# Performance work log

Hardware: AMD Instinct MI355X
Metric: run time of the kernel (lower is better)

The kernel has to match this reference:

```python
import jax, jax.numpy as jnp
import numpy as np

TOP_K = 2
SCALING = 16.0 / 8.0  # alpha / rank


def setup_inputs() -> dict:
    key = jax.random.key(0)
    ks = jax.random.split(key, 9)
    B, V, D, P = 32, 21, 512, 64
    IN, OUT, E, R, H = D * P, 96, 8, 8, 256
    return {
        "x": jax.random.normal(ks[0], (B, V, D, P), jnp.float32),
        "W_base": jax.random.normal(ks[1], (OUT, IN), jnp.float32) * (IN ** -0.5),
        "b_base": jax.random.normal(ks[2], (OUT,), jnp.float32) * 0.01,
        "W1": jax.random.normal(ks[3], (H, D), jnp.float32) * (D ** -0.5),
        "b1": jax.random.normal(ks[4], (H,), jnp.float32) * 0.01,
        "W2": jax.random.normal(ks[5], (E, H), jnp.float32) * (H ** -0.5),
        "b2": jax.random.normal(ks[6], (E,), jnp.float32) * 0.01,
        "lora_A": jax.random.normal(ks[7], (E, R, IN), jnp.float32) * (IN ** -0.5),
        "lora_B": jax.random.normal(ks[8], (E, OUT, R), jnp.float32) * (R ** -0.5),
    }


def reference(x, W_base, b_base, W1, b1, W2, b2, lora_A, lora_B):
    B, V, D, P = x.shape
    E = lora_A.shape[0]
    # FlattenHead: flatten last two dims, then linear (dropout is identity in eval)
    flat = x.reshape(B, V, D * P)                      # [B, V, IN]
    base_out = flat @ W_base.T + b_base                # [B, V, OUT]
    # Router: pool over n_vars then patch dim -> [B, D]
    pooled = x.mean(axis=1).mean(axis=-1)
    h = jax.nn.relu(pooled @ W1.T + b1)
    logits = h @ W2.T + b2                             # [B, E]
    probs = jax.nn.softmax(logits, axis=-1)
    topw, topi = jax.lax.top_k(probs, TOP_K)           # [B, K]
    topw = topw / jnp.clip(topw.sum(-1, keepdims=True), 1e-6)
    # All LoRA experts (matches original dense compute), then weighted combine
    temp = jnp.einsum("bvi,eri->ebvr", flat, lora_A)   # [E, B, V, R]
    delta = jnp.einsum("ebvr,eor->ebvo", temp, lora_B) * SCALING  # [E, B, V, OUT]
    # Scatter top-k weights into dense [B, E] then combine (top-k sparse combine)
    w_full = jnp.zeros((B, E), x.dtype).at[jnp.arange(B)[:, None], topi].add(topw)
    moe_delta = jnp.einsum("be,ebvo->bvo", w_full, delta)
    return base_out + moe_delta, probs
```

## Files before the change

kernel.cpp:

```cpp
#include <hip/hip_runtime.h>

#define B_DIM 32
#define V_DIM 21
#define D_DIM 512
#define P_DIM 64
#define M_TOTAL 672
#define K_TOTAL 32768
#define OUT_DIM 96
#define E_DIM 8
#define R_DIM 8
#define H_DIM 256
#define N_TOTAL 160
#define SCALING 2.0f
#define POOL_SCALE (1.0f / (V_DIM * (float)P_DIM))

#define BM 64
#define BK 64
#define KSPLIT 64
#define K_PER_SPLIT (K_TOTAL / KSPLIT)
#define CHUNKS (K_PER_SPLIT / BK)
#define LDS_K (BK + 8)
#define SMN (M_TOTAL * N_TOTAL)
#define RC_ROWS 2

typedef __attribute__((ext_vector_type(4))) float floatx4;
typedef __attribute__((ext_vector_type(8))) short short8;
typedef __attribute__((ext_vector_type(4))) short shortx4;

__device__ __forceinline__ unsigned short f2bf(float f) {
  union { float f; unsigned int u; } v; v.f = f;
  unsigned int u = v.u + (0x7FFFu + ((v.u >> 16) & 1u));
  return (unsigned short)(u >> 16);
}

__global__ __launch_bounds__(256)
void convW_kernel(const float* __restrict__ W_base, const float* __restrict__ lora_A,
                  short* __restrict__ Wb, float* __restrict__ pooled) {
  int gid = blockIdx.x * 256 + threadIdx.x;
  if (blockIdx.x < 64) pooled[gid] = 0.0f;
  size_t base = (size_t)gid * 8;
  int row = (int)(base >> 15);
  int k = (int)(base & 32767);
  const float* src = (row < OUT_DIM) ? (W_base + ((size_t)row << 15) + k)
                                     : (lora_A + ((size_t)(row - OUT_DIM) << 15) + k);
  floatx4 v0 = ((const floatx4*)src)[0];
  floatx4 v1 = ((const floatx4*)src)[1];
  short8 sv;
  sv[0] = (short)f2bf(v0[0]); sv[1] = (short)f2bf(v0[1]);
  sv[2] = (short)f2bf(v0[2]); sv[3] = (short)f2bf(v0[3]);
  sv[4] = (short)f2bf(v1[0]); sv[5] = (short)f2bf(v1[1]);
  sv[6] = (short)f2bf(v1[2]); sv[7] = (short)f2bf(v1[3]);
  *(short8*)(Wb + base) = sv;
}

__global__ __launch_bounds__(256, 4)
void gemm_kernel(const float* __restrict__ x, const short* __restrict__ Wb,
                 float* __restrict__ P, float* __restrict__ pooled) {
  __shared__ short ldsA[BM * LDS_K];
  __shared__ short ldsB[N_TOTAL * LDS_K];
  __shared__ float lds_pool[5 * 8];
  const int tid = threadIdx.x;
  const int m0 = blockIdx.x * BM;
  const int ky = blockIdx.y;
  const int kbase = ky * K_PER_SPLIT;
  const int lane = tid & 63;
  const int wave = tid >> 6;
  const int quad = lane >> 4;
  const int l16 = lane & 15;
  const int b_first = m0 / V_DIM;
  const int d_first = kbase >> 6;

  if (tid < 40) lds_pool[tid] = 0.0f;

  floatx4 acc[10];
  #pragma unroll
  for (int nt = 0; nt < 10; ++nt) acc[nt] = (floatx4)(0.0f);

  floatx4 pa[4];
  short8 pb[5];

#define ISSUE(c)                                                                \
  {                                                                             \
    const int kc = kbase + (c) * BK;                                            \
    _Pragma("unroll")                                                           \
    for (int it = 0; it < 4; ++it) {                                            \
      int idx = it * 256 + tid;                                                 \
      int arow = idx >> 4;                                                      \
      int u = idx & 15;                                                         \
      int m = m0 + arow;                                                        \
      pa[it] = (m < M_TOTAL)                                                    \
          ? *(const floatx4*)(x + (size_t)m * K_TOTAL + kc + u * 4)             \
          : (floatx4)(0.0f);                                                    \
    }                                                                           \
    _Pragma("unroll")                                                           \
    for (int it = 0; it < 5; ++it) {                                            \
      int idx = it * 256 + tid;                                                 \
      int brow = idx >> 3;                                                      \
      int g = idx & 7;                                                          \
      pb[it] = *(const short8*)(Wb + (size_t)brow * K_TOTAL + kc + g * 8);      \
    }                                                                           \
  }

#define CONVERT_WRITE(c)                                                        \
  {                                                                             \
    _Pragma("unroll")                                                           \
    for (int it = 0; it < 4; ++it) {                                            \
      int idx = it * 256 + tid;                                                 \
      int arow = idx >> 4;                                                      \
      int u = idx & 15;                                                         \
      int m = m0 + arow;                                                        \
      floatx4 v = pa[it];                                                       \
         \
      float s = (v[0] + v[1]) + (v[2] + v[3]);                                  \
      s += __shfl_down(s, 8, 16);                                               \
      s += __shfl_down(s, 4, 16);                                               \
      s += __shfl_down(s, 2, 16);                                               \
      s += __shfl_down(s, 1, 16);                                               \
      if ((tid & 15) == 0 && m < M_TOTAL) {                                     \
        int b_local = (m / V_DIM) - b_first;                                    \
        atomicAdd(&lds_pool[b_local * 8 + (c)], s);                             \
      }                                                                         \
      shortx4 sv;                                                               \
      sv[0] = (short)f2bf(v[0]); sv[1] = (short)f2bf(v[1]);                     \
      sv[2] = (short)f2bf(v[2]); sv[3] = (short)f2bf(v[3]);                     \
      *(shortx4*)&ldsA[arow * LDS_K + u * 4] = sv;                              \
    }                                                                           \
    _Pragma("unroll")                                                           \
    for (int it = 0; it < 5; ++it) {                                            \
      int idx = it * 256 + tid;                                                 \
      int brow = idx >> 3;                                                      \
      int g = idx & 7;                                                          \
      *(short8*)&ldsB[brow * LDS_K + g * 8] = pb[it];                           \
    }                                                                           \
  }

  ISSUE(0);
  __syncthreads();
  CONVERT_WRITE(0);

  for (int c = 0; c < CHUNKS; ++c) {
    __syncthreads();
    if (c + 1 < CHUNKS) ISSUE(c + 1);
    #pragma unroll
    for (int ks = 0; ks < 2; ++ks) {
      const int ko = ks * 32 + quad * 8;
      short8 a = *(const short8*)&ldsA[(wave * 16 + l16) * LDS_K + ko];
      #pragma unroll
      for (int nt = 0; nt < 10; ++nt) {
        short8 b = *(const short8*)&ldsB[(nt * 16 + l16) * LDS_K + ko];
        acc[nt] = __builtin_amdgcn_mfma_f32_16x16x32_bf16(a, b, acc[nt], 0, 0, 0);
      }
    }
    __syncthreads();
    if (c + 1 < CHUNKS) CONVERT_WRITE(c + 1);
  }

  {
    const int mrow = m0 + wave * 16 + quad * 4;
    float* Pp = P + (size_t)ky * SMN + (size_t)mrow * N_TOTAL + l16;
    #pragma unroll
    for (int r = 0; r < 4; ++r)
      if (mrow + r < M_TOTAL)
        #pragma unroll
        for (int nt = 0; nt < 10; ++nt)
          Pp[(size_t)r * N_TOTAL + nt * 16] = acc[nt][r];
  }

  if (tid < 40) {
    int b = b_first + (tid >> 3);
    int d = d_first + (tid & 7);
    if (b < B_DIM)
      atomicAdd(&pooled[b * D_DIM + d], lds_pool[tid] * POOL_SCALE);
  }
}

__global__ __launch_bounds__(256)
void router_kernel(const float* __restrict__ pooled, const float* __restrict__ W1,
                   const float* __restrict__ b1, const float* __restrict__ W2,
                   const float* __restrict__ b2, float* __restrict__ wfull,
                   float* __restrict__ probs_out) {
  __shared__ float sp[D_DIM];
  __shared__ float sh[H_DIM];
  __shared__ float slog[E_DIM];
  const int b = blockIdx.x;
  const int t = threadIdx.x;
  sp[t] = pooled[b * D_DIM + t];
  sp[t + 256] = pooled[b * D_DIM + t + 256];
  __syncthreads();
  float acc = b1[t];
  const float* w1r = W1 + (size_t)t * D_DIM;
  for (int d = 0; d < D_DIM; ++d) acc += sp[d] * w1r[d];
  sh[t] = fmaxf(acc, 0.0f);
  __syncthreads();
  if (t < E_DIM) {
    float a = b2[t];
    const float* w2r = W2 + t * H_DIM;
    for (int j = 0; j < H_DIM; ++j) a += sh[j] * w2r[j];
    slog[t] = a;
  }
  __syncthreads();
  if (t == 0) {
    float p[E_DIM];
    float mx = slog[0];
    for (int e = 1; e < E_DIM; ++e) mx = fmaxf(mx, slog[e]);
    float se = 0.0f;
    for (int e = 0; e < E_DIM; ++e) { p[e] = __expf(slog[e] - mx); se += p[e]; }
    float inv = 1.0f / se;
    for (int e = 0; e < E_DIM; ++e) { p[e] *= inv; probs_out[b * E_DIM + e] = p[e]; }
    int i0 = 0;
    for (int e = 1; e < E_DIM; ++e) if (p[e] > p[i0]) i0 = e;
    int i1 = (i0 == 0) ? 1 : 0;
    for (int e = 0; e < E_DIM; ++e) if (e != i0 && p[e] > p[i1]) i1 = e;
    float s2 = p[i0] + p[i1];
    float invs = 1.0f / fmaxf(s2, 1e-6f);
    for (int e = 0; e < E_DIM; ++e) {
      float w = 0.0f;
      if (e == i0) w += p[i0] * invs;
      if (e == i1) w += p[i1] * invs;
      wfull[b * E_DIM + e] = w;
    }
  }
}

__global__ __launch_bounds__(256)
void reduce_combine_kernel(const float* __restrict__ P, const float* __restrict__ b_base,
                           const float* __restrict__ lora_B, const float* __restrict__ wfull,
                           float* __restrict__ out) {
  __shared__ float sS[RC_ROWS * N_TOTAL];
  const int t = threadIdx.x;
  const size_t base = (size_t)blockIdx.x * (RC_ROWS * N_TOTAL);
  for (int s = t; s < RC_ROWS * N_TOTAL; s += 256) {
    const float* Pp = P + base + s;
    float a = 0.0f;
    #pragma unroll 8
    for (int k = 0; k < KSPLIT; ++k) a += Pp[(size_t)k * SMN];
    sS[s] = a;
  }
  __syncthreads();
  if (t < RC_ROWS * OUT_DIM) {
    int mr = t / OUT_DIM;
    int o = t - mr * OUT_DIM;
    int mm = blockIdx.x * RC_ROWS + mr;
    int b = mm / V_DIM;
    const float* srow = sS + mr * N_TOTAL;
    float res = srow[o] + b_base[o];
    float moe = 0.0f;
    #pragma unroll
    for (int e = 0; e < E_DIM; ++e) {
      float we = wfull[b * E_DIM + e];
      if (we != 0.0f) {
        const float* lb = lora_B + ((size_t)e * OUT_DIM + o) * R_DIM;
        float dd = 0.0f;
        #pragma unroll
        for (int r = 0; r < R_DIM; ++r) dd += srow[OUT_DIM + e * R_DIM + r] * lb[r];
        moe += we * dd;
      }
    }
    out[(size_t)mm * OUT_DIM + o] = res + SCALING * moe;
  }
}

extern "C" void kernel_launch(void* const* d_in, const int* in_sizes, int n_in,
                              void* d_out, int out_size, void* d_ws, size_t ws_size,
                              hipStream_t stream) {
  const float* x      = (const float*)d_in[0];
  const float* W_base = (const float*)d_in[1];
  const float* b_base = (const float*)d_in[2];
  const float* W1     = (const float*)d_in[3];
  const float* b1     = (const float*)d_in[4];
  const float* W2     = (const float*)d_in[5];
  const float* b2     = (const float*)d_in[6];
  const float* lora_A = (const float*)d_in[7];
  const float* lora_B = (const float*)d_in[8];
  float* out = (float*)d_out;

  float* ws     = (float*)d_ws;
  float* pooled = ws;
  float* wfull  = ws + 16384;
  short* Wb     = (short*)(wfull + 256);
  float* P      = (float*)(Wb + (size_t)N_TOTAL * K_TOTAL);

  convW_kernel<<<(N_TOTAL * K_TOTAL / 8 + 255) / 256, 256, 0, stream>>>(
      W_base, lora_A, Wb, pooled);
  gemm_kernel<<<dim3(11, KSPLIT), 256, 0, stream>>>(x, Wb, P, pooled);
  router_kernel<<<B_DIM, 256, 0, stream>>>(pooled, W1, b1, W2, b2, wfull,
                                           out + (size_t)M_TOTAL * OUT_DIM);
  reduce_combine_kernel<<<M_TOTAL / RC_ROWS, 256, 0, stream>>>(
      P, b_base, lora_B, wfull, out);
}
```

Before: 205.5 us.

## Pre-convert x to bf16 in a separate pass and move pooling out of GEMM

Adds a combined conversion kernel that turns x into a bf16 workspace copy and computes the router's pooled means with atomics, alongside the existing weight conversion. The GEMM then loads bf16 x directly, with no in-loop conversion or pooling reduction, and the router now runs before the GEMM. This makes the GEMM main loop simpler and halves its A-operand load bytes. In exchange it adds an extra write and re-read of a bf16 copy of x, plus a memset.

```diff
diff --git a/kernel.cpp b/kernel.cpp
--- a/kernel.cpp
+++ b/kernel.cpp
@@ -23,9 +23,11 @@
 #define SMN (M_TOTAL * N_TOTAL)
 #define RC_ROWS 2
 
+#define XCONV_BLOCKS 10752
+#define WCONV_BLOCKS 2560
+
 typedef __attribute__((ext_vector_type(4))) float floatx4;
 typedef __attribute__((ext_vector_type(8))) short short8;
-typedef __attribute__((ext_vector_type(4))) short shortx4;
 
 __device__ __forceinline__ unsigned short f2bf(float f) {
   union { float f; unsigned int u; } v; v.f = f;
@@ -34,31 +36,55 @@
 }
 
 __global__ __launch_bounds__(256)
-void convW_kernel(const float* __restrict__ W_base, const float* __restrict__ lora_A,
-                  short* __restrict__ Wb, float* __restrict__ pooled) {
-  int gid = blockIdx.x * 256 + threadIdx.x;
-  if (blockIdx.x < 64) pooled[gid] = 0.0f;
-  size_t base = (size_t)gid * 8;
-  int row = (int)(base >> 15);
-  int k = (int)(base & 32767);
-  const float* src = (row < OUT_DIM) ? (W_base + ((size_t)row << 15) + k)
-                                     : (lora_A + ((size_t)(row - OUT_DIM) << 15) + k);
-  floatx4 v0 = ((const floatx4*)src)[0];
-  floatx4 v1 = ((const floatx4*)src)[1];
-  short8 sv;
-  sv[0] = (short)f2bf(v0[0]); sv[1] = (short)f2bf(v0[1]);
-  sv[2] = (short)f2bf(v0[2]); sv[3] = (short)f2bf(v0[3]);
-  sv[4] = (short)f2bf(v1[0]); sv[5] = (short)f2bf(v1[1]);
-  sv[6] = (short)f2bf(v1[2]); sv[7] = (short)f2bf(v1[3]);
-  *(short8*)(Wb + base) = sv;
+void conv_kernel(const float* __restrict__ x, const float* __restrict__ W_base,
+                 const float* __restrict__ lora_A, short* __restrict__ xb,
+                 short* __restrict__ Wb, float* __restrict__ pooled) {
+  const int tid = threadIdx.x;
+  if (blockIdx.x < XCONV_BLOCKS) {
+    size_t gid = (size_t)blockIdx.x * 256 + tid;
+    const int m = (int)(gid >> 12);
+    const int grp = (int)(gid & 4095);
+    const float* src = x + ((size_t)m << 15) + grp * 8;
+    floatx4 v0 = ((const floatx4*)src)[0];
+    floatx4 v1 = ((const floatx4*)src)[1];
+    short8 sv;
+    sv[0] = (short)f2bf(v0[0]); sv[1] = (short)f2bf(v0[1]);
+    sv[2] = (short)f2bf(v0[2]); sv[3] = (short)f2bf(v0[3]);
+    sv[4] = (short)f2bf(v1[0]); sv[5] = (short)f2bf(v1[1]);
+    sv[6] = (short)f2bf(v1[2]); sv[7] = (short)f2bf(v1[3]);
+    *(short8*)(xb + gid * 8) = sv;
+    float s = ((v0[0] + v0[1]) + (v0[2] + v0[3])) +
+              ((v1[0] + v1[1]) + (v1[2] + v1[3]));
+    s += __shfl_down(s, 4, 8);
+    s += __shfl_down(s, 2, 8);
+    s += __shfl_down(s, 1, 8);
+    if ((tid & 7) == 0) {
+      int b = m / V_DIM;
+      int d = grp >> 3;
+      atomicAdd(&pooled[b * D_DIM + d], s * POOL_SCALE);
+    }
+  } else {
+    size_t base = ((size_t)(blockIdx.x - XCONV_BLOCKS) * 256 + tid) * 8;
+    int row = (int)(base >> 15);
+    int k = (int)(base & 32767);
+    const float* src = (row < OUT_DIM) ? (W_base + ((size_t)row << 15) + k)
+                                       : (lora_A + ((size_t)(row - OUT_DIM) << 15) + k);
+    floatx4 v0 = ((const floatx4*)src)[0];
+    floatx4 v1 = ((const floatx4*)src)[1];
+    short8 sv;
+    sv[0] = (short)f2bf(v0[0]); sv[1] = (short)f2bf(v0[1]);
+    sv[2] = (short)f2bf(v0[2]); sv[3] = (short)f2bf(v0[3]);
+    sv[4] = (short)f2bf(v1[0]); sv[5] = (short)f2bf(v1[1]);
+    sv[6] = (short)f2bf(v1[2]); sv[7] = (short)f2bf(v1[3]);
+    *(short8*)(Wb + base) = sv;
+  }
 }
 
 __global__ __launch_bounds__(256, 4)
-void gemm_kernel(const float* __restrict__ x, const short* __restrict__ Wb,
-                 float* __restrict__ P, float* __restrict__ pooled) {
+void gemm_kernel(const short* __restrict__ xb, const short* __restrict__ Wb,
+                 float* __restrict__ P) {
   __shared__ short ldsA[BM * LDS_K];
   __shared__ short ldsB[N_TOTAL * LDS_K];
-  __shared__ float lds_pool[5 * 8];
   const int tid = threadIdx.x;
   const int m0 = blockIdx.x * BM;
   const int ky = blockIdx.y;
@@ -67,63 +93,44 @@
   const int wave = tid >> 6;
   const int quad = lane >> 4;
   const int l16 = lane & 15;
-  const int b_first = m0 / V_DIM;
-  const int d_first = kbase >> 6;
-
-  if (tid < 40) lds_pool[tid] = 0.0f;
 
   floatx4 acc[10];
   #pragma unroll
   for (int nt = 0; nt < 10; ++nt) acc[nt] = (floatx4)(0.0f);
 
-  floatx4 pa[4];
+  short8 pa[2];
   short8 pb[5];
 
 #define ISSUE(c)                                                                \
   {                                                                             \
     const int kc = kbase + (c) * BK;                                            \
     _Pragma("unroll")                                                           \
-    for (int it = 0; it < 4; ++it) {                                            \
-      int idx = it * 256 + tid;                                                 \
-      int arow = idx >> 4;                                                      \
-      int u = idx & 15;                                                         \
+    for (int it = 0; it < 2; ++it) {                                            \
+      int idx = it * 256 + tid;                                                 \
+      int arow = idx >> 3;                                                      \
+      int g = idx & 7;                                                          \
       int m = m0 + arow;                                                        \
       pa[it] = (m < M_TOTAL)                                                    \
-          ? *(const floatx4*)(x + (size_t)m * K_TOTAL + kc + u * 4)             \
-          : (floatx4)(0.0f);                                                    \
+          ? *(const short8*)(xb + ((size_t)m << 15) + kc + g * 8)               \
+          : (short8)(0);                                                        \
     }                                                                           \
     _Pragma("unroll")                                                           \
     for (int it = 0; it < 5; ++it) {                                            \
       int idx = it * 256 + tid;                                                 \
       int brow = idx >> 3;                                                      \
       int g = idx & 7;                                                          \
-      pb[it] = *(const short8*)(Wb + (size_t)brow * K_TOTAL + kc + g * 8);      \
-    }                                                                           \
-  }
-
-#define CONVERT_WRITE(c)                                                        \
+      pb[it] = *(const short8*)(Wb + ((size_t)brow << 15) + kc + g * 8);        \
+    }                                                                           \
+  }
+
+#define WRITE_LDS()                                                             \
   {                                                                             \
     _Pragma("unroll")                                                           \
-    for (int it = 0; it < 4; ++it) {                                            \
-      int idx = it * 256 + tid;                                                 \
-      int arow = idx >> 4;                                                      \
-      int u = idx & 15;                                                         \
-      int m = m0 + arow;                                                        \
-      floatx4 v = pa[it];                                                       \
-         \
-      float s = (v[0] + v[1]) + (v[2] + v[3]);                                  \
-      s += __shfl_down(s, 8, 16);                                               \
-      s += __shfl_down(s, 4, 16);                                               \
-      s += __shfl_down(s, 2, 16);                                               \
-      s += __shfl_down(s, 1, 16);                                               \
-      if ((tid & 15) == 0 && m < M_TOTAL) {                                     \
-        int b_local = (m / V_DIM) - b_first;                                    \
-        atomicAdd(&lds_pool[b_local * 8 + (c)], s);                             \
-      }                                                                         \
-      shortx4 sv;                                                               \
-      sv[0] = (short)f2bf(v[0]); sv[1] = (short)f2bf(v[1]);                     \
-      sv[2] = (short)f2bf(v[2]); sv[3] = (short)f2bf(v[3]);                     \
-      *(shortx4*)&ldsA[arow * LDS_K + u * 4] = sv;                              \
+    for (int it = 0; it < 2; ++it) {                                            \
+      int idx = it * 256 + tid;                                                 \
+      int arow = idx >> 3;                                                      \
+      int g = idx & 7;                                                          \
+      *(short8*)&ldsA[arow * LDS_K + g * 8] = pa[it];                           \
     }                                                                           \
     _Pragma("unroll")                                                           \
     for (int it = 0; it < 5; ++it) {                                            \
@@ -135,8 +142,7 @@
   }
 
   ISSUE(0);
-  __syncthreads();
-  CONVERT_WRITE(0);
+  WRITE_LDS();
 
   for (int c = 0; c < CHUNKS; ++c) {
     __syncthreads();
@@ -152,7 +158,7 @@
       }
     }
     __syncthreads();
-    if (c + 1 < CHUNKS) CONVERT_WRITE(c + 1);
+    if (c + 1 < CHUNKS) WRITE_LDS();
   }
 
   {
@@ -164,13 +170,6 @@
         #pragma unroll
         for (int nt = 0; nt < 10; ++nt)
           Pp[(size_t)r * N_TOTAL + nt * 16] = acc[nt][r];
-  }
-
-  if (tid < 40) {
-    int b = b_first + (tid >> 3);
-    int d = d_first + (tid & 7);
-    if (b < B_DIM)
-      atomicAdd(&pooled[b * D_DIM + d], lds_pool[tid] * POOL_SCALE);
   }
 }
 
@@ -278,13 +277,15 @@
   float* pooled = ws;
   float* wfull  = ws + 16384;
   short* Wb     = (short*)(wfull + 256);
-  float* P      = (float*)(Wb + (size_t)N_TOTAL * K_TOTAL);
-
-  convW_kernel<<<(N_TOTAL * K_TOTAL / 8 + 255) / 256, 256, 0, stream>>>(
-      W_base, lora_A, Wb, pooled);
-  gemm_kernel<<<dim3(11, KSPLIT), 256, 0, stream>>>(x, Wb, P, pooled);
+  short* xb     = Wb + (size_t)N_TOTAL * K_TOTAL;
+  float* P      = (float*)(xb + (size_t)M_TOTAL * K_TOTAL);
+
+  (void)hipMemsetAsync(pooled, 0, 16384 * sizeof(float), stream);
+  conv_kernel<<<XCONV_BLOCKS + WCONV_BLOCKS, 256, 0, stream>>>(
+      x, W_base, lora_A, xb, Wb, pooled);
   router_kernel<<<B_DIM, 256, 0, stream>>>(pooled, W1, b1, W2, b2, wfull,
                                            out + (size_t)M_TOTAL * OUT_DIM);
+  gemm_kernel<<<dim3(11, KSPLIT), 256, 0, stream>>>(xb, Wb, P);
   reduce_combine_kernel<<<M_TOTAL / RC_ROWS, 256, 0, stream>>>(
       P, b_base, lora_B, wfull, out);
 }
```

After: 215.5 us. +4.9%, slower.
